# Kernel tuning notes

Hardware: AMD Instinct MI355X
Metric: run time of the kernel (lower is better)

The kernel has to match this reference:

```python
import jax, jax.numpy as jnp
import numpy as np

CTRL, WORD, MEM, D_IN = 256, 128, 128, 64
B, T = 512, 512
EPS = 1e-6


def setup_inputs() -> dict:
    key = jax.random.key(0)
    ks = jax.random.split(key, 16)
    rs = np.random.RandomState(0)

    data = jax.random.normal(ks[0], (T, B, D_IN), dtype=jnp.float32)

    # ragged lengths -> packed-style batch_sizes (descending, batch_sizes[0]=B)
    lengths = rs.randint(T // 2, T + 1, size=B)
    batch_sizes = jnp.asarray((lengths[None, :] > np.arange(T)[:, None]).sum(1),
                              dtype=jnp.int32)  # [T]
    unsort_idxs = jnp.asarray(rs.permutation(B), dtype=jnp.int32)

    sc = 0.02
    p = lambda k, sh: sc * jax.random.normal(k, sh, dtype=jnp.float32)
    return {
        "data": data,
        "batch_sizes": batch_sizes,
        "unsort_idxs": unsort_idxs,
        # GRU controller: input = D_IN + WORD, hidden = CTRL
        "W_ih": p(ks[1], (3 * CTRL, D_IN + WORD)),
        "b_ih": jnp.zeros((3 * CTRL,), jnp.float32),
        "W_hh": p(ks[2], (3 * CTRL, CTRL)),
        "b_hh": jnp.zeros((3 * CTRL,), jnp.float32),
        # memory head projections (from ctrl_out)
        "W_key": p(ks[3], (WORD, CTRL)), "b_key": jnp.zeros((WORD,), jnp.float32),
        "W_beta": p(ks[4], (1, CTRL)), "b_beta": jnp.zeros((1,), jnp.float32),
        "W_erase": p(ks[5], (WORD, CTRL)), "b_erase": jnp.zeros((WORD,), jnp.float32),
        "W_add": p(ks[6], (WORD, CTRL)), "b_add": jnp.zeros((WORD,), jnp.float32),
        # learned initial memory, shared across batch
        "M0": p(ks[7], (MEM, WORD)),
    }


def _gru(x, h, W_ih, b_ih, W_hh, b_hh):
    gi = x @ W_ih.T + b_ih          # [b, 3*CTRL]
    gh = h @ W_hh.T + b_hh
    ir, iz, inn = jnp.split(gi, 3, axis=-1)
    hr, hz, hn = jnp.split(gh, 3, axis=-1)
    r = jax.nn.sigmoid(ir + hr)
    z = jax.nn.sigmoid(iz + hz)
    n = jnp.tanh(inn + r * hn)
    return (1.0 - z) * n + z * h


def _memory(ctrl, M, W_key, b_key, W_beta, b_beta, W_erase, b_erase, W_add, b_add):
    # content addressing
    k = jnp.tanh(ctrl @ W_key.T + b_key)                       # [b, WORD]
    beta = jax.nn.softplus(ctrl @ W_beta.T + b_beta)           # [b, 1]
    Mn = M / (jnp.linalg.norm(M, axis=-1, keepdims=True) + EPS)
    kn = k / (jnp.linalg.norm(k, axis=-1, keepdims=True) + EPS)
    cos = jnp.einsum('bmw,bw->bm', Mn, kn)                     # [b, MEM]
    w = jax.nn.softmax(beta * cos, axis=-1)                    # [b, MEM]
    read = jnp.einsum('bm,bmw->bw', w, M)                      # [b, WORD]
    # erase/add write
    e = jax.nn.sigmoid(ctrl @ W_erase.T + b_erase)             # [b, WORD]
    a = ctrl @ W_add.T + b_add                                 # [b, WORD]
    M_new = M * (1.0 - w[:, :, None] * e[:, None, :]) + w[:, :, None] * a[:, None, :]
    return read, M_new


def reference(data, batch_sizes, unsort_idxs,
              W_ih, b_ih, W_hh, b_hh,
              W_key, b_key, W_beta, b_beta,
              W_erase, b_erase, W_add, b_add, M0):
    row = jnp.arange(B)

    def step(carry, inp):
        ctrl, read, M = carry
        x_t, size = inp
        active = (row < size)[:, None]                          # [B,1]
        ctrl_in = jnp.concatenate((x_t, read), axis=1)          # [B, D_IN+WORD]
        ctrl_new = _gru(ctrl_in, ctrl, W_ih, b_ih, W_hh, b_hh)
        read_new, M_new = _memory(ctrl_new, M, W_key, b_key, W_beta, b_beta,
                                  W_erase, b_erase, W_add, b_add)
        # inactive rows keep their final state (packed-batch semantics)
        ctrl = jnp.where(active, ctrl_new, ctrl)
        read = jnp.where(active, read_new, read)
        M = jnp.where(active[:, :, None], M_new, M)
        return (ctrl, read, M), None

    init = (jnp.zeros((B, CTRL), data.dtype),
            jnp.zeros((B, WORD), data.dtype),
            jnp.broadcast_to(M0, (B, MEM, WORD)))
    (ctrl, read, _), _ = jax.lax.scan(step, init, (data, batch_sizes))
    return ctrl[unsort_idxs], read[unsort_idxs]
```

## Files before the change

### kernel.cpp

```cpp
#include <hip/hip_runtime.h>
#include <math.h>

#define NB 512
#define NT 512
#define NCTRL 256
#define NWORD 128
#define NMEM 128
#define NDIN 64
#define NACT 448
#define EPSF 1e-6f

#define H_WA   0
#define H_WNI  229376
#define H_WNH  278528
#define H_WH   344064
#define H_TOTAL 475136
#define B_BA   0
#define B_BNI  512
#define B_BNH  768
#define B_BH   1024
#define B_TOTAL 1536
#define WS_BYTES (H_TOTAL * 2 + B_TOTAL * 4)

typedef _Float16 h2 __attribute__((ext_vector_type(2)));
typedef _Float16 h8 __attribute__((ext_vector_type(8)));
union H8 { h8 v; h2 d[4]; };

__device__ __forceinline__ float sigf(float x) { return 1.0f / (1.0f + expf(-x)); }
__device__ __forceinline__ float softplusf(float x) {
    return (x > 15.0f) ? x : log1pf(expf(x));
}
__device__ __forceinline__ float fdot2(h2 a, h2 b, float c) {
#if __has_builtin(__builtin_amdgcn_fdot2)
    return __builtin_amdgcn_fdot2(a, b, c, false);
#else
    return fmaf((float)a[0], (float)b[0], fmaf((float)a[1], (float)b[1], c));
#endif
}

__global__ __launch_bounds__(256) void prep_kernel(
    const float* __restrict__ Wih, const float* __restrict__ bih,
    const float* __restrict__ Whh, const float* __restrict__ bhh,
    const float* __restrict__ Wkey, const float* __restrict__ bkey,
    const float* __restrict__ Wbeta, const float* __restrict__ bbeta,
    const float* __restrict__ Wer, const float* __restrict__ ber,
    const float* __restrict__ Wadd, const float* __restrict__ badd,
    _Float16* __restrict__ wsH, float* __restrict__ wsB)
{
    int i = blockIdx.x * 256 + threadIdx.x;
    if (i < H_TOTAL) {
        float v;
        if (i < H_WNI) {
            int ch = i >> 3, e = i & 7;
            int kc = ch >> 9, col = ch & 511;
            int k = kc * 8 + e;
            v = (k < 192) ? Wih[col * 192 + k] : Whh[col * 256 + (k - 192)];
        } else if (i < H_WNH) {
            int i2 = i - H_WNI; int ch = i2 >> 3, e = i2 & 7;
            int kc = ch >> 8, col = ch & 255;
            v = Wih[(512 + col) * 192 + kc * 8 + e];
        } else if (i < H_WH) {
            int i2 = i - H_WNH; int ch = i2 >> 3, e = i2 & 7;
            int kc = ch >> 8, col = ch & 255;
            v = Whh[(512 + col) * 256 + kc * 8 + e];
        } else {
            int i2 = i - H_WH; int ch = i2 >> 3, e = i2 & 7;
            int kc = ch >> 9, col = ch & 511;
            int k = kc * 8 + e;
            if (col < 128)       v = Wkey[col * 256 + k];
            else if (col < 256)  v = Wer[(col - 128) * 256 + k];
            else if (col < 384)  v = Wadd[(col - 256) * 256 + k];
            else if (col == 384) v = Wbeta[k];
            else                 v = 0.0f;
        }
        wsH[i] = (_Float16)v;
    } else if (i < H_TOTAL + B_TOTAL) {
        int j = i - H_TOTAL;
        float v;
        if (j < 512)        v = bih[j] + bhh[j];
        else if (j < 768)   v = bih[512 + (j - 512)];
        else if (j < 1024)  v = bhh[512 + (j - 768)];
        else {
            int c = j - 1024;
            if (c < 128)       v = bkey[c];
            else if (c < 256)  v = ber[c - 128];
            else if (c < 384)  v = badd[c - 256];
            else if (c == 384) v = bbeta[0];
            else               v = 0.0f;
        }
        wsB[j] = v;
    }
}

__device__ __forceinline__ void memory_step(
    int u, bool wr, float (*M)[NWORD + 1],
    const float* keyv, const float* ev, const float* av,
    float* cosb, float* wb, float* part, float* readv, float* scal)
{
    if (u < 64) {
        float s = keyv[u] * keyv[u] + keyv[u + 64] * keyv[u + 64];
        #pragma unroll
        for (int o = 32; o >= 1; o >>= 1) s += __shfl_xor(s, o);
        if (u == 0) scal[0] = 1.0f / (sqrtf(s) + EPSF);
    }
    __syncthreads();
    {
        int rr = u >> 1, hh = u & 1;
        const float* Mr = &M[rr][hh * 64];
        const float4* kk4 = (const float4*)(keyv + hh * 64);
        float s2 = 0.f, sc = 0.f;
        #pragma unroll
        for (int p = 0; p < 16; ++p) {
            float4 k4 = kk4[p];
            float m0 = Mr[4 * p], m1 = Mr[4 * p + 1], m2 = Mr[4 * p + 2], m3 = Mr[4 * p + 3];
            s2 = fmaf(m0, m0, s2); sc = fmaf(m0, k4.x, sc);
            s2 = fmaf(m1, m1, s2); sc = fmaf(m1, k4.y, sc);
            s2 = fmaf(m2, m2, s2); sc = fmaf(m2, k4.z, sc);
            s2 = fmaf(m3, m3, s2); sc = fmaf(m3, k4.w, sc);
        }
        s2 += __shfl_xor(s2, 1);
        sc += __shfl_xor(sc, 1);
        if (hh == 0) cosb[rr] = sc * scal[0] / (sqrtf(s2) + EPSF);
    }
    __syncthreads();
    if (u < 64) {
        float beta = scal[1];
        float l0 = beta * cosb[u], l1 = beta * cosb[u + 64];
        float mx = fmaxf(l0, l1);
        #pragma unroll
        for (int o = 32; o >= 1; o >>= 1) mx = fmaxf(mx, __shfl_xor(mx, o));
        float e0 = expf(l0 - mx), e1 = expf(l1 - mx);
        float s = e0 + e1;
        #pragma unroll
        for (int o = 32; o >= 1; o >>= 1) s += __shfl_xor(s, o);
        float inv = 1.0f / s;
        wb[u] = e0 * inv;
        wb[u + 64] = e1 * inv;
    }
    __syncthreads();
    {
        int j = u & 127, rh = u >> 7;
        float ej = ev[j], aj = av[j];
        const float4* wb4 = (const float4*)(wb + rh * 64);
        float p = 0.f;
        #pragma unroll
        for (int pq = 0; pq < 16; ++pq) {
            float4 w4 = wb4[pq];
            int r = rh * 64 + 4 * pq;
            float m0 = M[r][j], m1 = M[r + 1][j], m2 = M[r + 2][j], m3 = M[r + 3][j];
            p = fmaf(w4.x, m0, p);
            p = fmaf(w4.y, m1, p);
            p = fmaf(w4.z, m2, p);
            p = fmaf(w4.w, m3, p);
            if (wr) {
                M[r][j]     = fmaf(-w4.x, fmaf(ej, m0, -aj), m0);
                M[r + 1][j] = fmaf(-w4.y, fmaf(ej, m1, -aj), m1);
                M[r + 2][j] = fmaf(-w4.z, fmaf(ej, m2, -aj), m2);
                M[r + 3][j] = fmaf(-w4.w, fmaf(ej, m3, -aj), m3);
            }
        }
        part[rh * 128 + j] = p;
    }
    __syncthreads();
    if (wr && u < 128) readv[u] = part[u] + part[128 + u];
}

__global__ __launch_bounds__(512) void ntm_fast2(
    const float* __restrict__ data, const int* __restrict__ batch_sizes,
    const int* __restrict__ unsort, const float* __restrict__ M0,
    const _Float16* __restrict__ wsH, const float* __restrict__ wsB,
    float* __restrict__ out)
{
    __shared__ float M[2][NMEM][NWORD + 1];
    __shared__ __align__(16) _Float16 actH[2][NACT];
    __shared__ float ctrlB[2][NCTRL];
    __shared__ float gA[2][512];
    __shared__ float iA[2][NCTRL];
    __shared__ float hA[2][NCTRL];
    __shared__ __align__(16) float readv[2][NWORD], keyv[2][NWORD], ev[2][NWORD], av[2][NWORD];
    __shared__ __align__(16) float cosb[2][NMEM], wb[2][NMEM], part[2][2 * NWORD], scal[2][2];
    __shared__ int len_sh[2], gpos[2];

    const int t = threadIdx.x;
    const int q = t >> 8;
    const int u = t & 255;
    const int g = blockIdx.x;
    const int b = 2 * g + q;

    if (t < 2) {
        int bb = 2 * g + t;
        int L = 0;
        for (int s = 0; s < NT; ++s) L += (batch_sizes[s] > bb);
        len_sh[t] = L;
    }
    {
        int ug = unsort[t];
        if (ug == 2 * g)     gpos[0] = t;
        if (ug == 2 * g + 1) gpos[1] = t;
    }
    for (int i = t; i < 2 * NMEM * NWORD; i += 512) {
        int ii = i & (NMEM * NWORD - 1);
        M[i >> 14][ii >> 7][ii & 127] = M0[ii];
    }
    ctrlB[q][u] = 0.0f;
    actH[q][192 + u] = (_Float16)0.0f;
    if (u < NWORD) readv[q][u] = 0.0f;
    __syncthreads();
    const int len0 = len_sh[0], len1 = len_sh[1];

    const float bRZ  = wsB[B_BA + t];
    const float bAux = (t < 256) ? wsB[B_BNI + u] : wsB[B_BNH + u];
    const float bHD  = wsB[B_BH + t];

    const h8* __restrict__ pA  = (const h8*)(wsH + H_WA);
    const h8* __restrict__ pI  = (const h8*)(wsH + H_WNI);
    const h8* __restrict__ pH  = (const h8*)(wsH + H_WNH);
    const h8* __restrict__ pHD = (const h8*)(wsH + H_WH);
    const h8* A0 = (const h8*)actH[0];
    const h8* A1 = (const h8*)actH[1];

    for (int ts = 0; ts < len0; ++ts) {
        const bool wr = (q == 0) | (ts < len1);
        if (u < 128)      actH[q][64 + u] = (_Float16)readv[q][u];
        else if (u < 192) actH[q][u - 128] =
            (_Float16)data[((long)ts * NB + b) * NDIN + (u - 128)];
        __syncthreads();

        float a0 = bRZ, c0 = 0.f, a1 = bRZ, c1 = 0.f;
        float e0 = bAux, f0 = 0.f, e1 = bAux, f1 = 0.f;
        if (t < 256) {
            #pragma unroll 4
            for (int kc = 0; kc < 24; ++kc) {
                H8 x0; x0.v = A0[kc];
                H8 x1; x1.v = A1[kc];
                H8 w;  w.v  = pA[kc * 512 + t];
                H8 wn; wn.v = pI[kc * 256 + u];
                a0 = fdot2(x0.d[0], w.d[0], a0);  c0 = fdot2(x0.d[1], w.d[1], c0);
                a0 = fdot2(x0.d[2], w.d[2], a0);  c0 = fdot2(x0.d[3], w.d[3], c0);
                a1 = fdot2(x1.d[0], w.d[0], a1);  c1 = fdot2(x1.d[1], w.d[1], c1);
                a1 = fdot2(x1.d[2], w.d[2], a1);  c1 = fdot2(x1.d[3], w.d[3], c1);
                e0 = fdot2(x0.d[0], wn.d[0], e0); f0 = fdot2(x0.d[1], wn.d[1], f0);
                e0 = fdot2(x0.d[2], wn.d[2], e0); f0 = fdot2(x0.d[3], wn.d[3], f0);
                e1 = fdot2(x1.d[0], wn.d[0], e1); f1 = fdot2(x1.d[1], wn.d[1], f1);
                e1 = fdot2(x1.d[2], wn.d[2], e1); f1 = fdot2(x1.d[3], wn.d[3], f1);
            }
            #pragma unroll 4
            for (int kc = 24; kc < 56; ++kc) {
                H8 x0; x0.v = A0[kc];
                H8 x1; x1.v = A1[kc];
                H8 w;  w.v  = pA[kc * 512 + t];
                a0 = fdot2(x0.d[0], w.d[0], a0);  c0 = fdot2(x0.d[1], w.d[1], c0);
                a0 = fdot2(x0.d[2], w.d[2], a0);  c0 = fdot2(x0.d[3], w.d[3], c0);
                a1 = fdot2(x1.d[0], w.d[0], a1);  c1 = fdot2(x1.d[1], w.d[1], c1);
                a1 = fdot2(x1.d[2], w.d[2], a1);  c1 = fdot2(x1.d[3], w.d[3], c1);
            }
        } else {
            #pragma unroll 4
            for (int kc = 0; kc < 24; ++kc) {
                H8 x0; x0.v = A0[kc];
                H8 x1; x1.v = A1[kc];
                H8 w;  w.v  = pA[kc * 512 + t];
                a0 = fdot2(x0.d[0], w.d[0], a0);  c0 = fdot2(x0.d[1], w.d[1], c0);
                a0 = fdot2(x0.d[2], w.d[2], a0);  c0 = fdot2(x0.d[3], w.d[3], c0);
                a1 = fdot2(x1.d[0], w.d[0], a1);  c1 = fdot2(x1.d[1], w.d[1], c1);
                a1 = fdot2(x1.d[2], w.d[2], a1);  c1 = fdot2(x1.d[3], w.d[3], c1);
            }
            #pragma unroll 4
            for (int kc = 24; kc < 56; ++kc) {
                H8 x0; x0.v = A0[kc];
                H8 x1; x1.v = A1[kc];
                H8 w;  w.v  = pA[kc * 512 + t];
                H8 wn; wn.v = pH[(kc - 24) * 256 + u];
                a0 = fdot2(x0.d[0], w.d[0], a0);  c0 = fdot2(x0.d[1], w.d[1], c0);
                a0 = fdot2(x0.d[2], w.d[2], a0);  c0 = fdot2(x0.d[3], w.d[3], c0);
                a1 = fdot2(x1.d[0], w.d[0], a1);  c1 = fdot2(x1.d[1], w.d[1], c1);
                a1 = fdot2(x1.d[2], w.d[2], a1);  c1 = fdot2(x1.d[3], w.d[3], c1);
                e0 = fdot2(x0.d[0], wn.d[0], e0); f0 = fdot2(x0.d[1], wn.d[1], f0);
                e0 = fdot2(x0.d[2], wn.d[2], e0); f0 = fdot2(x0.d[3], wn.d[3], f0);
                e1 = fdot2(x1.d[0], wn.d[0], e1); f1 = fdot2(x1.d[1], wn.d[1], f1);
                e1 = fdot2(x1.d[2], wn.d[2], e1); f1 = fdot2(x1.d[3], wn.d[3], f1);
            }
        }
        gA[0][t] = a0 + c0;
        gA[1][t] = a1 + c1;
        if (t < 256) { iA[0][u] = e0 + f0; iA[1][u] = e1 + f1; }
        else         { hA[0][u] = e0 + f0; hA[1][u] = e1 + f1; }
        __syncthreads();

        {
            float rg = sigf(gA[q][u]);
            float zg = sigf(gA[q][NCTRL + u]);
            float ng = tanhf(fmaf(rg, hA[q][u], iA[q][u]));
            float cold = ctrlB[q][u];
            float cnew = fmaf(zg, cold - ng, ng);
            if (wr) {
                ctrlB[q][u] = cnew;
                actH[q][192 + u] = (_Float16)cnew;
            }
        }
        __syncthreads();

        float h0 = bHD, d0 = 0.f, h1 = bHD, d1 = 0.f;
        #pragma unroll 4
        for (int kc = 0; kc < 32; ++kc) {
            H8 x0; x0.v = A0[24 + kc];
            H8 x1; x1.v = A1[24 + kc];
            H8 w;  w.v  = pHD[kc * 512 + t];
            h0 = fdot2(x0.d[0], w.d[0], h0);  d0 = fdot2(x0.d[1], w.d[1], d0);
            h0 = fdot2(x0.d[2], w.d[2], h0);  d0 = fdot2(x0.d[3], w.d[3], d0);
            h1 = fdot2(x1.d[0], w.d[0], h1);  d1 = fdot2(x1.d[1], w.d[1], d1);
            h1 = fdot2(x1.d[2], w.d[2], h1);  d1 = fdot2(x1.d[3], w.d[3], d1);
        }
        h0 += d0; h1 += d1;
        if (t < 128)       { keyv[0][t] = tanhf(h0);      keyv[1][t] = tanhf(h1); }
        else if (t < 256)  { ev[0][t - 128] = sigf(h0);   ev[1][t - 128] = sigf(h1); }
        else if (t < 384)  { av[0][t - 256] = h0;         av[1][t - 256] = h1; }
        else if (t == 384) { scal[0][1] = softplusf(h0);  scal[1][1] = softplusf(h1); }
        __syncthreads();

        memory_step(u, wr, M[q], keyv[q], ev[q], av[q],
                    cosb[q], wb[q], part[q], readv[q], scal[q]);
    }

    out[gpos[q] * NCTRL + u] = ctrlB[q][u];
    if (u < NWORD) out[NB * NCTRL + gpos[q] * NWORD + u] = readv[q][u];
}

__global__ __launch_bounds__(256) void ntm_slow(
    const float* __restrict__ data, const int* __restrict__ batch_sizes,
    const int* __restrict__ unsort,
    const float* __restrict__ Wih, const float* __restrict__ bih,
    const float* __restrict__ Whh, const float* __restrict__ bhh,
    const float* __restrict__ Wkey, const float* __restrict__ bkey,
    const float* __restrict__ Wbeta, const float* __restrict__ bbeta,
    const float* __restrict__ Wer, const float* __restrict__ ber,
    const float* __restrict__ Wadd, const float* __restrict__ badd,
    const float* __restrict__ M0, float* __restrict__ out)
{
    __shared__ float M[NMEM][NWORD + 1];
    __shared__ float act[NACT];
    __shared__ float ctrlB[NCTRL];
    __shared__ float gpre[512], ginn[256], ghn[256], hpre[448];
    __shared__ __align__(16) float readv[NWORD], keyv[NWORD], ev[NWORD], av[NWORD];
    __shared__ __align__(16) float cosb[NMEM], wb[NMEM], part[2 * NWORD], scal[2];
    __shared__ int len_sh;

    const int tid = threadIdx.x;
    const int g = blockIdx.x;
    const int b = unsort[g];

    if (tid == 0) {
        int L = 0;
        for (int t = 0; t < NT; ++t) L += (batch_sizes[t] > b);
        len_sh = L;
    }
    for (int i = tid; i < NMEM * NWORD; i += 256)
        M[i >> 7][i & 127] = M0[i];
    ctrlB[tid] = 0.0f;
    if (tid < NWORD) readv[tid] = 0.0f;
    __syncthreads();
    const int len = len_sh;
    const int wave = tid >> 6, lane = tid & 63;

    for (int t = 0; t < len; ++t) {
        if (tid < 64)  act[tid] = data[((long)t * NB + b) * NDIN + tid];
        if (tid < 128) act[64 + tid] = readv[tid];
        act[192 + tid] = ctrlB[tid];
        __syncthreads();

        for (int j = wave; j < 512; j += 4) {
            float p = 0.f;
            for (int k = lane; k < 192; k += 64) p = fmaf(act[k], Wih[j * 192 + k], p);
            for (int k = lane; k < 256; k += 64) p = fmaf(act[192 + k], Whh[j * 256 + k], p);
            #pragma unroll
            for (int o = 32; o >= 1; o >>= 1) p += __shfl_xor(p, o);
            if (lane == 0) gpre[j] = p;
        }
        for (int j = wave; j < 256; j += 4) {
            float pi = 0.f, ph = 0.f;
            for (int k = lane; k < 192; k += 64) pi = fmaf(act[k], Wih[(512 + j) * 192 + k], pi);
            for (int k = lane; k < 256; k += 64) ph = fmaf(act[192 + k], Whh[(512 + j) * 256 + k], ph);
            #pragma unroll
            for (int o = 32; o >= 1; o >>= 1) { pi += __shfl_xor(pi, o); ph += __shfl_xor(ph, o); }
            if (lane == 0) { ginn[j] = pi; ghn[j] = ph; }
        }
        __syncthreads();
        {
            float r = sigf(gpre[tid] + bih[tid] + bhh[tid]);
            float z = sigf(gpre[256 + tid] + bih[256 + tid] + bhh[256 + tid]);
            float inn = ginn[tid] + bih[512 + tid];
            float hn  = ghn[tid] + bhh[512 + tid];
            float n = tanhf(fmaf(r, hn, inn));
            float cold = act[192 + tid];
            ctrlB[tid] = fmaf(z, cold - n, n);
        }
        __syncthreads();
        for (int j = wave; j < 385; j += 4) {
            const float* Wp; long base;
            if (j < 128)      { Wp = Wkey;  base = (long)j * 256; }
            else if (j < 256) { Wp = Wer;   base = (long)(j - 128) * 256; }
            else if (j < 384) { Wp = Wadd;  base = (long)(j - 256) * 256; }
            else              { Wp = Wbeta; base = 0; }
            float p = 0.f;
            for (int k = lane; k < 256; k += 64) p = fmaf(ctrlB[k], Wp[base + k], p);
            #pragma unroll
            for (int o = 32; o >= 1; o >>= 1) p += __shfl_xor(p, o);
            if (lane == 0) hpre[j] = p;
        }
        __syncthreads();
        if (tid < 128) {
            keyv[tid] = tanhf(hpre[tid] + bkey[tid]);
            ev[tid]   = sigf(hpre[128 + tid] + ber[tid]);
            av[tid]   = hpre[256 + tid] + badd[tid];
        }
        if (tid == 0) scal[1] = softplusf(hpre[384] + bbeta[0]);
        __syncthreads();

        memory_step(tid, true, M, keyv, ev, av, cosb, wb, part, readv, scal);
        __syncthreads();
    }

    out[g * NCTRL + tid] = ctrlB[tid];
    if (tid < NWORD) out[NB * NCTRL + g * NWORD + tid] = readv[tid];
}

extern "C" void kernel_launch(void* const* d_in, const int* in_sizes, int n_in,
                              void* d_out, int out_size, void* d_ws, size_t ws_size,
                              hipStream_t stream)
{
    const float* data       = (const float*)d_in[0];
    const int*  batch_sizes = (const int*)d_in[1];
    const int*  unsort      = (const int*)d_in[2];
    float* out = (float*)d_out;

    if (ws_size >= (size_t)WS_BYTES) {
        _Float16* wsH = (_Float16*)d_ws;
        float* wsB = (float*)((char*)d_ws + (size_t)H_TOTAL * 2);
        prep_kernel<<<(H_TOTAL + B_TOTAL + 255) / 256, 256, 0, stream>>>(
            (const float*)d_in[3], (const float*)d_in[4], (const float*)d_in[5],
            (const float*)d_in[6], (const float*)d_in[7], (const float*)d_in[8],
            (const float*)d_in[9], (const float*)d_in[10], (const float*)d_in[11],
            (const float*)d_in[12], (const float*)d_in[13], (const float*)d_in[14],
            wsH, wsB);
        ntm_fast2<<<NB / 2, 512, 0, stream>>>(data, batch_sizes, unsort,
                                              (const float*)d_in[15], wsH, wsB, out);
    } else {
        ntm_slow<<<NB, 256, 0, stream>>>(
            data, batch_sizes, unsort,
            (const float*)d_in[3], (const float*)d_in[4], (const float*)d_in[5],
            (const float*)d_in[6], (const float*)d_in[7], (const float*)d_in[8],
            (const float*)d_in[9], (const float*)d_in[10], (const float*)d_in[11],
            (const float*)d_in[12], (const float*)d_in[13], (const float*)d_in[14],
            (const float*)d_in[15], out);
    }
}
```

Measured before the change: 6.721 ms.

## Prefetch next-step weights into registers and inline memory step with lighter barriers

Loads the first weight chunks and next-timestep input into registers during the softmax/memory phase, hiding global-load latency behind the serial recurrence. Replaces __syncthreads with an LDS-only waitcnt+barrier so outstanding global prefetches need not drain at each barrier. The memory step is inlined with the key norm computed via wave shuffles during the head projection and a two-thread-per-row cosine reduction. It also raises register pressure (launch_bounds 512,2) and risks spills.

Result: slower. 21.52 ms (+220.2%).

```diff
diff --git a/kernel.cpp b/kernel.cpp
--- a/kernel.cpp
+++ b/kernel.cpp
@@ -22,6 +22,10 @@
 #define B_TOTAL 1536
 #define WS_BYTES (H_TOTAL * 2 + B_TOTAL * 4)
 
+#define PFA 16
+#define PFX 8
+#define PFH 8
+
 typedef _Float16 h2 __attribute__((ext_vector_type(2)));
 typedef _Float16 h8 __attribute__((ext_vector_type(8)));
 union H8 { h8 v; h2 d[4]; };
@@ -36,6 +40,10 @@
 #else
     return fmaf((float)a[0], (float)b[0], fmaf((float)a[1], (float)b[1], c));
 #endif
+}
+
+__device__ __forceinline__ void barL() {
+    asm volatile("s_waitcnt lgkmcnt(0)\n\ts_barrier" ::: "memory");
 }
 
 __global__ __launch_bounds__(256) void prep_kernel(
@@ -165,7 +173,41 @@
     if (wr && u < 128) readv[u] = part[u] + part[128 + u];
 }
 
-__global__ __launch_bounds__(512) void ntm_fast2(
+#define DOT_RZ(WSRC) do { H8 w_; w_.v = (WSRC); \
+    a0 = fdot2(x0.d[0], w_.d[0], a0); c0 = fdot2(x0.d[1], w_.d[1], c0); \
+    a0 = fdot2(x0.d[2], w_.d[2], a0); c0 = fdot2(x0.d[3], w_.d[3], c0); \
+    a1 = fdot2(x1.d[0], w_.d[0], a1); c1 = fdot2(x1.d[1], w_.d[1], c1); \
+    a1 = fdot2(x1.d[2], w_.d[2], a1); c1 = fdot2(x1.d[3], w_.d[3], c1); } while (0)
+
+#define DOT_AUX(WSRC) do { H8 w_; w_.v = (WSRC); \
+    e0 = fdot2(x0.d[0], w_.d[0], e0); f0 = fdot2(x0.d[1], w_.d[1], f0); \
+    e0 = fdot2(x0.d[2], w_.d[2], e0); f0 = fdot2(x0.d[3], w_.d[3], f0); \
+    e1 = fdot2(x1.d[0], w_.d[0], e1); f1 = fdot2(x1.d[1], w_.d[1], f1); \
+    e1 = fdot2(x1.d[2], w_.d[2], e1); f1 = fdot2(x1.d[3], w_.d[3], f1); } while (0)
+
+#define DOT_HD(WSRC) do { H8 w_; w_.v = (WSRC); \
+    h0 = fdot2(x0.d[0], w_.d[0], h0); d0 = fdot2(x0.d[1], w_.d[1], d0); \
+    h0 = fdot2(x0.d[2], w_.d[2], h0); d0 = fdot2(x0.d[3], w_.d[3], d0); \
+    h1 = fdot2(x1.d[0], w_.d[0], h1); d1 = fdot2(x1.d[1], w_.d[1], d1); \
+    h1 = fdot2(x1.d[2], w_.d[2], h1); d1 = fdot2(x1.d[3], w_.d[3], d1); } while (0)
+
+#define LOADX(KC) H8 x0; x0.v = A0[KC]; H8 x1; x1.v = A1[KC]
+
+#define ISSUE_SWEEP_PF(TS) do { \
+    int tn_ = ((TS) < NT) ? (TS) : 0; \
+    if (u >= 128 && u < 192) xf = data[((long)tn_ * NB + b) * NDIN + (u - 128)]; \
+    _Pragma("unroll") \
+    for (int i_ = 0; i_ < PFA; ++i_) pfA[i_] = pA[i_ * 512 + t]; \
+    if (t < 256) { \
+        _Pragma("unroll") \
+        for (int i_ = 0; i_ < PFX; ++i_) pfX[i_] = pI[i_ * 256 + u]; \
+    } else { \
+        _Pragma("unroll") \
+        for (int i_ = 0; i_ < PFX; ++i_) pfX[i_] = pH[i_ * 256 + u]; \
+    } \
+} while (0)
+
+__global__ __launch_bounds__(512, 2) void ntm_fast3(
     const float* __restrict__ data, const int* __restrict__ batch_sizes,
     const int* __restrict__ unsort, const float* __restrict__ M0,
     const _Float16* __restrict__ wsH, const float* __restrict__ wsB,
@@ -178,7 +220,8 @@
     __shared__ float iA[2][NCTRL];
     __shared__ float hA[2][NCTRL];
     __shared__ __align__(16) float readv[2][NWORD], keyv[2][NWORD], ev[2][NWORD], av[2][NWORD];
-    __shared__ __align__(16) float cosb[2][NMEM], wb[2][NMEM], part[2][2 * NWORD], scal[2][2];
+    __shared__ __align__(16) float cosb[2][NMEM], wb[2][NMEM], part[2][2 * NWORD];
+    __shared__ float kn2[2][2], betav[2];
     __shared__ int len_sh[2], gpos[2];
 
     const int t = threadIdx.x;
@@ -219,73 +262,71 @@
     const h8* A0 = (const h8*)actH[0];
     const h8* A1 = (const h8*)actH[1];
 
+    h8 pfA[PFA];
+    h8 pfX[PFX];
+    float xf = 0.0f;
+    ISSUE_SWEEP_PF(0);
+
     for (int ts = 0; ts < len0; ++ts) {
         const bool wr = (q == 0) | (ts < len1);
         if (u < 128)      actH[q][64 + u] = (_Float16)readv[q][u];
-        else if (u < 192) actH[q][u - 128] =
-            (_Float16)data[((long)ts * NB + b) * NDIN + (u - 128)];
-        __syncthreads();
+        else if (u < 192) actH[q][u - 128] = (_Float16)xf;
+        barL();
 
         float a0 = bRZ, c0 = 0.f, a1 = bRZ, c1 = 0.f;
         float e0 = bAux, f0 = 0.f, e1 = bAux, f1 = 0.f;
         if (t < 256) {
-            #pragma unroll 4
-            for (int kc = 0; kc < 24; ++kc) {
-                H8 x0; x0.v = A0[kc];
-                H8 x1; x1.v = A1[kc];
-                H8 w;  w.v  = pA[kc * 512 + t];
-                H8 wn; wn.v = pI[kc * 256 + u];
-                a0 = fdot2(x0.d[0], w.d[0], a0);  c0 = fdot2(x0.d[1], w.d[1], c0);
-                a0 = fdot2(x0.d[2], w.d[2], a0);  c0 = fdot2(x0.d[3], w.d[3], c0);
-                a1 = fdot2(x1.d[0], w.d[0], a1);  c1 = fdot2(x1.d[1], w.d[1], c1);
-                a1 = fdot2(x1.d[2], w.d[2], a1);  c1 = fdot2(x1.d[3], w.d[3], c1);
-                e0 = fdot2(x0.d[0], wn.d[0], e0); f0 = fdot2(x0.d[1], wn.d[1], f0);
-                e0 = fdot2(x0.d[2], wn.d[2], e0); f0 = fdot2(x0.d[3], wn.d[3], f0);
-                e1 = fdot2(x1.d[0], wn.d[0], e1); f1 = fdot2(x1.d[1], wn.d[1], f1);
-                e1 = fdot2(x1.d[2], wn.d[2], e1); f1 = fdot2(x1.d[3], wn.d[3], f1);
+            #pragma unroll
+            for (int kc = 0; kc < PFX; ++kc) {
+                LOADX(kc);
+                DOT_RZ(pfA[kc]); DOT_AUX(pfX[kc]);
+            }
+            #pragma unroll
+            for (int kc = PFX; kc < PFA; ++kc) {
+                LOADX(kc);
+                DOT_RZ(pfA[kc]); DOT_AUX(pI[kc * 256 + u]);
+            }
+            #pragma unroll
+            for (int kc = PFA; kc < 24; ++kc) {
+                LOADX(kc);
+                DOT_RZ(pA[kc * 512 + t]); DOT_AUX(pI[kc * 256 + u]);
             }
             #pragma unroll 4
             for (int kc = 24; kc < 56; ++kc) {
-                H8 x0; x0.v = A0[kc];
-                H8 x1; x1.v = A1[kc];
-                H8 w;  w.v  = pA[kc * 512 + t];
-                a0 = fdot2(x0.d[0], w.d[0], a0);  c0 = fdot2(x0.d[1], w.d[1], c0);
-                a0 = fdot2(x0.d[2], w.d[2], a0);  c0 = fdot2(x0.d[3], w.d[3], c0);
-                a1 = fdot2(x1.d[0], w.d[0], a1);  c1 = fdot2(x1.d[1], w.d[1], c1);
-                a1 = fdot2(x1.d[2], w.d[2], a1);  c1 = fdot2(x1.d[3], w.d[3], c1);
+                LOADX(kc);
+                DOT_RZ(pA[kc * 512 + t]);
             }
         } else {
+            #pragma unroll
+            for (int kc = 0; kc < PFA; ++kc) {
+                LOADX(kc);
+                DOT_RZ(pfA[kc]);
+            }
+            #pragma unroll
+            for (int kc = PFA; kc < 24; ++kc) {
+                LOADX(kc);
+                DOT_RZ(pA[kc * 512 + t]);
+            }
+            #pragma unroll
+            for (int kc = 24; kc < 24 + PFX; ++kc) {
+                LOADX(kc);
+                DOT_RZ(pA[kc * 512 + t]); DOT_AUX(pfX[kc - 24]);
+            }
             #pragma unroll 4
-            for (int kc = 0; kc < 24; ++kc) {
-                H8 x0; x0.v = A0[kc];
-                H8 x1; x1.v = A1[kc];
-                H8 w;  w.v  = pA[kc * 512 + t];
-                a0 = fdot2(x0.d[0], w.d[0], a0);  c0 = fdot2(x0.d[1], w.d[1], c0);
-                a0 = fdot2(x0.d[2], w.d[2], a0);  c0 = fdot2(x0.d[3], w.d[3], c0);
-                a1 = fdot2(x1.d[0], w.d[0], a1);  c1 = fdot2(x1.d[1], w.d[1], c1);
-                a1 = fdot2(x1.d[2], w.d[2], a1);  c1 = fdot2(x1.d[3], w.d[3], c1);
-            }
-            #pragma unroll 4
-            for (int kc = 24; kc < 56; ++kc) {
-                H8 x0; x0.v = A0[kc];
-                H8 x1; x1.v = A1[kc];
-                H8 w;  w.v  = pA[kc * 512 + t];
-                H8 wn; wn.v = pH[(kc - 24) * 256 + u];
-                a0 = fdot2(x0.d[0], w.d[0], a0);  c0 = fdot2(x0.d[1], w.d[1], c0);
-                a0 = fdot2(x0.d[2], w.d[2], a0);  c0 = fdot2(x0.d[3], w.d[3], c0);
-                a1 = fdot2(x1.d[0], w.d[0], a1);  c1 = fdot2(x1.d[1], w.d[1], c1);
-                a1 = fdot2(x1.d[2], w.d[2], a1);  c1 = fdot2(x1.d[3], w.d[3], c1);
-                e0 = fdot2(x0.d[0], wn.d[0], e0); f0 = fdot2(x0.d[1], wn.d[1], f0);
-                e0 = fdot2(x0.d[2], wn.d[2], e0); f0 = fdot2(x0.d[3], wn.d[3], f0);
-                e1 = fdot2(x1.d[0], wn.d[0], e1); f1 = fdot2(x1.d[1], wn.d[1], f1);
-                e1 = fdot2(x1.d[2], wn.d[2], e1); f1 = fdot2(x1.d[3], wn.d[3], f1);
-            }
-        }
+            for (int kc = 24 + PFX; kc < 56; ++kc) {
+                LOADX(kc);
+                DOT_RZ(pA[kc * 512 + t]); DOT_AUX(pH[(kc - 24) * 256 + u]);
+            }
+        }
+        h8 pfHd[PFH];
+        #pragma unroll
+        for (int i = 0; i < PFH; ++i) pfHd[i] = pHD[i * 512 + t];
+
         gA[0][t] = a0 + c0;
         gA[1][t] = a1 + c1;
         if (t < 256) { iA[0][u] = e0 + f0; iA[1][u] = e1 + f1; }
         else         { hA[0][u] = e0 + f0; hA[1][u] = e1 + f1; }
-        __syncthreads();
+        barL();
 
         {
             float rg = sigf(gA[q][u]);
@@ -298,28 +339,99 @@
                 actH[q][192 + u] = (_Float16)cnew;
             }
         }
-        __syncthreads();
+        barL();
 
         float h0 = bHD, d0 = 0.f, h1 = bHD, d1 = 0.f;
+        #pragma unroll
+        for (int kc = 0; kc < PFH; ++kc) {
+            LOADX(24 + kc);
+            DOT_HD(pfHd[kc]);
+        }
         #pragma unroll 4
-        for (int kc = 0; kc < 32; ++kc) {
-            H8 x0; x0.v = A0[24 + kc];
-            H8 x1; x1.v = A1[24 + kc];
-            H8 w;  w.v  = pHD[kc * 512 + t];
-            h0 = fdot2(x0.d[0], w.d[0], h0);  d0 = fdot2(x0.d[1], w.d[1], d0);
-            h0 = fdot2(x0.d[2], w.d[2], h0);  d0 = fdot2(x0.d[3], w.d[3], d0);
-            h1 = fdot2(x1.d[0], w.d[0], h1);  d1 = fdot2(x1.d[1], w.d[1], d1);
-            h1 = fdot2(x1.d[2], w.d[2], h1);  d1 = fdot2(x1.d[3], w.d[3], d1);
+        for (int kc = PFH; kc < 32; ++kc) {
+            LOADX(24 + kc);
+            DOT_HD(pHD[kc * 512 + t]);
         }
         h0 += d0; h1 += d1;
-        if (t < 128)       { keyv[0][t] = tanhf(h0);      keyv[1][t] = tanhf(h1); }
-        else if (t < 256)  { ev[0][t - 128] = sigf(h0);   ev[1][t - 128] = sigf(h1); }
-        else if (t < 384)  { av[0][t - 256] = h0;         av[1][t - 256] = h1; }
-        else if (t == 384) { scal[0][1] = softplusf(h0);  scal[1][1] = softplusf(h1); }
-        __syncthreads();
-
-        memory_step(u, wr, M[q], keyv[q], ev[q], av[q],
-                    cosb[q], wb[q], part[q], readv[q], scal[q]);
+        if (t < 128) {
+            float k0 = tanhf(h0), k1 = tanhf(h1);
+            keyv[0][t] = k0; keyv[1][t] = k1;
+            float s0 = k0 * k0, s1 = k1 * k1;
+            #pragma unroll
+            for (int o = 32; o >= 1; o >>= 1) {
+                s0 += __shfl_xor(s0, o);
+                s1 += __shfl_xor(s1, o);
+            }
+            if ((t & 63) == 0) { kn2[0][t >> 6] = s0; kn2[1][t >> 6] = s1; }
+        }
+        else if (t < 256)  { ev[0][t - 128] = sigf(h0); ev[1][t - 128] = sigf(h1); }
+        else if (t < 384)  { av[0][t - 256] = h0;       av[1][t - 256] = h1; }
+        else if (t == 384) { betav[0] = softplusf(h0);  betav[1] = softplusf(h1); }
+        barL();
+
+        {
+            float invk = 1.0f / (sqrtf(kn2[q][0] + kn2[q][1]) + EPSF);
+            int rr = u >> 1, hh = u & 1;
+            const float* Mr = &M[q][rr][hh * 64];
+            const float4* kk4 = (const float4*)(&keyv[q][hh * 64]);
+            float s2 = 0.f, sc = 0.f;
+            #pragma unroll
+            for (int p = 0; p < 16; ++p) {
+                float4 k4 = kk4[p];
+                float m0 = Mr[4 * p], m1 = Mr[4 * p + 1], m2 = Mr[4 * p + 2], m3 = Mr[4 * p + 3];
+                s2 = fmaf(m0, m0, s2); sc = fmaf(m0, k4.x, sc);
+                s2 = fmaf(m1, m1, s2); sc = fmaf(m1, k4.y, sc);
+                s2 = fmaf(m2, m2, s2); sc = fmaf(m2, k4.z, sc);
+                s2 = fmaf(m3, m3, s2); sc = fmaf(m3, k4.w, sc);
+            }
+            s2 += __shfl_xor(s2, 1);
+            sc += __shfl_xor(sc, 1);
+            if (hh == 0) cosb[q][rr] = sc * invk / (sqrtf(s2) + EPSF);
+        }
+        barL();
+
+        if (u < 64) {
+            float beta = betav[q];
+            float l0 = beta * cosb[q][u], l1 = beta * cosb[q][u + 64];
+            float mx = fmaxf(l0, l1);
+            #pragma unroll
+            for (int o = 32; o >= 1; o >>= 1) mx = fmaxf(mx, __shfl_xor(mx, o));
+            float se0 = expf(l0 - mx), se1 = expf(l1 - mx);
+            float s = se0 + se1;
+            #pragma unroll
+            for (int o = 32; o >= 1; o >>= 1) s += __shfl_xor(s, o);
+            float inv = 1.0f / s;
+            wb[q][u] = se0 * inv;
+            wb[q][u + 64] = se1 * inv;
+        }
+        ISSUE_SWEEP_PF(ts + 1);
+        barL();
+
+        {
+            int j = u & 127, rh = u >> 7;
+            float ej = ev[q][j], aj = av[q][j];
+            const float4* wb4 = (const float4*)(&wb[q][rh * 64]);
+            float p = 0.f;
+            #pragma unroll
+            for (int pq = 0; pq < 16; ++pq) {
+                float4 w4 = wb4[pq];
+                int r = rh * 64 + 4 * pq;
+                float m0 = M[q][r][j], m1 = M[q][r + 1][j], m2 = M[q][r + 2][j], m3 = M[q][r + 3][j];
+                p = fmaf(w4.x, m0, p);
+                p = fmaf(w4.y, m1, p);
+                p = fmaf(w4.z, m2, p);
+                p = fmaf(w4.w, m3, p);
+                if (wr) {
+                    M[q][r][j]     = fmaf(-w4.x, fmaf(ej, m0, -aj), m0);
+                    M[q][r + 1][j] = fmaf(-w4.y, fmaf(ej, m1, -aj), m1);
+                    M[q][r + 2][j] = fmaf(-w4.z, fmaf(ej, m2, -aj), m2);
+                    M[q][r + 3][j] = fmaf(-w4.w, fmaf(ej, m3, -aj), m3);
+                }
+            }
+            part[q][rh * 128 + j] = p;
+        }
+        barL();
+        if (wr && u < 128) readv[q][u] = part[q][u] + part[q][128 + u];
     }
 
     out[gpos[q] * NCTRL + u] = ctrlB[q][u];
@@ -442,7 +554,7 @@
             (const float*)d_in[9], (const float*)d_in[10], (const float*)d_in[11],
             (const float*)d_in[12], (const float*)d_in[13], (const float*)d_in[14],
             wsH, wsB);
-        ntm_fast2<<<NB / 2, 512, 0, stream>>>(data, batch_sizes, unsort,
+        ntm_fast3<<<NB / 2, 512, 0, stream>>>(data, batch_sizes, unsort,
                                               (const float*)d_in[15], wsH, wsB, out);
     } else {
         ntm_slow<<<NB, 256, 0, stream>>>(
```
